# Kernel optimization log

Measured on AMD Instinct MI355X. Metric: run time of the kernel, lower is better.

The kernel has to match this reference:

```python
import math
import jax, jax.numpy as jnp
import numpy as np
from jax.scipy.special import erf

BATCH, SEQ, DIM = 2, 4096, 128
EMA_HEADS, DQK, DV = 16, 64, 256
NUM_BUCKETS, MAX_DIST = 32, 128


def _next_fast_len(n):
    # smallest 5-smooth integer >= n (matches scipy.fftpack.next_fast_len)
    while True:
        m = n
        for p in (2, 3, 5):
            while m % p == 0:
                m //= p
        if m == 1:
            return n
        n += 1


def _laplacian_attn(x):
    mu = math.sqrt(0.5)
    std = math.sqrt(0.25 * math.pi)
    return 0.5 * (1.0 + erf((x - mu) / (std * math.sqrt(2.0))))


def _rel_pos_bias(table, n, scale):
    # causal T5 relative position bias, bucket(q_pos - k_pos)
    pos = jnp.arange(n)
    rel = jnp.maximum(pos[:, None] - pos[None, :], 0)  # [n, n], >= 0
    max_exact = NUM_BUCKETS // 2
    is_small = rel < max_exact
    val_large = max_exact + (
        jnp.log(jnp.maximum(rel, 1).astype(jnp.float32) / max_exact)
        / math.log(MAX_DIST / max_exact) * (NUM_BUCKETS - max_exact)
    ).astype(jnp.int32)
    val_large = jnp.minimum(val_large, NUM_BUCKETS - 1)
    bucket = jnp.where(is_small, rel, val_large)
    return table[bucket, 0] * scale  # [n, n]


def _conv1d_fft(x, K, n):
    # x: [b, n, h, d] (fft over axis 1), K: [n, h] (fft over axis 0)
    fast_len = _next_fast_len(2 * n - 1)
    f_x = jnp.fft.rfft(x, n=fast_len, axis=1)
    f_K = jnp.fft.rfft(K, n=fast_len, axis=0)
    out = jnp.fft.irfft(f_x * jnp.conj(f_K)[None, :, :, None], fast_len, axis=1)
    out = jnp.roll(out, -1, axis=1)
    return out[:, fast_len - n:]  # [b, n, h, d]


def _forward(x, expansion, reduction, alphas, dampen, Wqk, bqk, gamma, beta,
             Wv, bv, rel_table, Wr, br, Wu, bu, Wh, Uh, bh):
    b, n, d = x.shape
    # ---- multi-headed EMA (causal -> unidirectional) via FFT conv ----
    xe = jnp.einsum('bnd,hd->bnhd', x, expansion)
    a = jax.nn.sigmoid(alphas)            # [h]
    dm = jax.nn.sigmoid(dampen)           # [h]
    powers = jnp.arange(n - 1, -1, -1, dtype=x.dtype)  # reversed powers
    K = a * ((1.0 - a) * dm) ** powers[:, None]        # [n, h]
    conv = _conv1d_fft(xe, K, n)
    ema = jnp.einsum('bnhd,hd->bnd', conv, reduction)  # [b, n, d]
    # ---- single-headed attention (chunk_size=-1 -> one chunk), v from x ----
    qk = jax.nn.silu(ema @ Wqk + bqk)     # [b, n, dqk]
    q = qk * gamma[0] + beta[0]
    k = qk * gamma[1] + beta[1]
    v = jax.nn.silu(x @ Wv + bv)          # [b, n, dv]
    scale = 1.0 / n                       # laplacian_attn_fn scaling
    sim = jnp.einsum('bid,bjd->bij', q, k) * scale
    sim = sim + _rel_pos_bias(rel_table, n, DQK ** 0.5)
    attn = _laplacian_attn(sim)
    causal_mask = jnp.triu(jnp.ones((n, n), dtype=bool), 1)
    attn = jnp.where(causal_mask, 0.0, attn)  # laplacian: zero after activation
    attn_out = jnp.einsum('bij,bjd->bid', attn, v)  # [b, n, dv]
    # ---- gating + output ----
    reset_gate = jax.nn.silu(ema @ Wr + br)         # [b, n, dv]
    update_gate = jax.nn.sigmoid(ema @ Wu + bu)     # [b, n, d]
    gated = attn_out * reset_gate
    H = jax.nn.silu(ema @ Wh + gated @ Uh + bh)     # [b, n, d]
    return update_gate * H + (1.0 - update_gate) * x


def setup_inputs() -> dict:
    key = jax.random.key(0)
    ks = jax.random.split(key, 18)
    def rn(i, shape, s=1.0):
        return jax.random.normal(ks[i], shape, dtype=jnp.float32) * s
    return dict(
        x=rn(0, (BATCH, SEQ, DIM)),
        expansion=rn(1, (EMA_HEADS, DIM), 0.2),
        reduction=rn(2, (EMA_HEADS, DIM), 0.2),
        alphas=rn(3, (EMA_HEADS,)),
        dampen=rn(4, (EMA_HEADS,)),
        Wqk=rn(5, (DIM, DQK), 0.05), bqk=rn(6, (DQK,), 0.02),
        gamma=rn(7, (2, DQK), 0.02), beta=jnp.zeros((2, DQK), jnp.float32),
        Wv=rn(8, (DIM, DV), 0.05), bv=rn(9, (DV,), 0.02),
        rel_table=rn(10, (NUM_BUCKETS, 1), 0.02),
        Wr=rn(11, (DIM, DV), 0.05), br=rn(12, (DV,), 0.02),
        Wu=rn(13, (DIM, DIM), 0.05), bu=rn(14, (DIM,), 0.02),
        Wh=rn(15, (DIM, DIM), 0.05), Uh=rn(16, (DV, DIM), 0.05),
        bh=rn(17, (DIM,), 0.02),
    )


def reference(x, expansion, reduction, alphas, dampen, Wqk, bqk, gamma, beta,
              Wv, bv, rel_table, Wr, br, Wu, bu, Wh, Uh, bh):
    return _forward(x, expansion, reduction, alphas, dampen, Wqk, bqk, gamma,
                    beta, Wv, bv, rel_table, Wr, br, Wu, bu, Wh, Uh, bh)
```

## Files before the change

kernel.cpp:

```cpp
#include <hip/hip_runtime.h>
#include <cstdint>
#include <cmath>

#define B_ 2
#define N_ 4096
#define D_ 128
#define H_ 16
#define DQK_ 64
#define DV_ 256

typedef float    f4_t  __attribute__((ext_vector_type(4)));
typedef float    f16f  __attribute__((ext_vector_type(16)));
typedef _Float16 h4_t  __attribute__((ext_vector_type(4)));
typedef _Float16 h8_t  __attribute__((ext_vector_type(8)));

__device__ __forceinline__ float sigmoidf_(float z) { return 1.f/(1.f + expf(-z)); }
__device__ __forceinline__ float siluf_(float z)    { return z/(1.f + expf(-z)); }
__device__ __forceinline__ f16f zero16() {
  f16f z;
#pragma unroll
  for (int i = 0; i < 16; ++i) z[i] = 0.f;
  return z;
}

__global__ void ema_phase1(const float* __restrict__ x, const float* __restrict__ expansion,
                           const float* __restrict__ alphas, const float* __restrict__ dampen,
                           float* __restrict__ F, _Float16* __restrict__ xh) {
  int bid = blockIdx.x;
  int dg = bid & 7, c = (bid >> 3) & 63, b = bid >> 9;
  int h = threadIdx.x & 15, dl = threadIdx.x >> 4;
  int d = dg*16 + dl;
  float a  = sigmoidf_(alphas[h]);
  float dm = sigmoidf_(dampen[h]);
  float q  = (1.f - a)*dm;
  float coef = a * expansion[h*D_ + d];
  __shared__ float xs[64][16];
  {
    int e = threadIdx.x;
    int t = e >> 2, seg = e & 3;
    const float* xp = x + ((size_t)b*N_ + c*64 + t)*D_ + dg*16 + seg*4;
    f4_t v = *(const f4_t*)xp;
    *(f4_t*)&xs[t][seg*4] = v;
    h4_t hv;
#pragma unroll
    for (int j = 0; j < 4; ++j) hv[j] = (_Float16)v[j];
    *(h4_t*)(xh + ((size_t)b*N_ + c*64 + t)*D_ + dg*16 + seg*4) = hv;
  }
  __syncthreads();
  float s = 0.f;
#pragma unroll
  for (int t = 0; t < 64; ++t) s = fmaf(q, s, coef*xs[t][dl]);
  F[(((size_t)b*H_ + h)*D_ + d)*64 + c] = s;
}

__global__ void ema_carry(const float* __restrict__ F, const float* __restrict__ alphas,
                          const float* __restrict__ dampen, float* __restrict__ carry) {
  int idx = blockIdx.x*256 + threadIdx.x;
  int h = (idx >> 7) & 15;
  float a  = sigmoidf_(alphas[h]);
  float dm = sigmoidf_(dampen[h]);
  float q  = (1.f - a)*dm;
  float qL = q;
#pragma unroll
  for (int i = 0; i < 6; ++i) qL *= qL;
  const float* Fp = F + (size_t)idx*64;
  float* cp = carry + (size_t)idx*64;
  float s = 0.f;
  for (int cc = 0; cc < 64; ++cc) { cp[cc] = s; s = fmaf(qL, s, Fp[cc]); }
}

__global__ void ema_phase2(const float* __restrict__ x, const float* __restrict__ expansion,
                           const float* __restrict__ reduction,
                           const float* __restrict__ alphas, const float* __restrict__ dampen,
                           const float* __restrict__ carry, _Float16* __restrict__ emah) {
  int bid = blockIdx.x;
  int dg = bid & 7, c = (bid >> 3) & 63, b = bid >> 9;
  int h = threadIdx.x & 15, dl = threadIdx.x >> 4;
  int d = dg*16 + dl;
  float a  = sigmoidf_(alphas[h]);
  float dm = sigmoidf_(dampen[h]);
  float q  = (1.f - a)*dm;
  float coef = a * expansion[h*D_ + d];
  float red  = reduction[h*D_ + d];
  __shared__ float xs[64][16];
  {
    int e = threadIdx.x;
    int t = e >> 2, seg = e & 3;
    const float* xp = x + ((size_t)b*N_ + c*64 + t)*D_ + dg*16 + seg*4;
    *(f4_t*)&xs[t][seg*4] = *(const f4_t*)xp;
  }
  __syncthreads();
  float s = carry[(((size_t)b*H_ + h)*D_ + d)*64 + c];
  for (int t = 0; t < 64; ++t) {
    s = fmaf(q, s, coef*xs[t][dl]);
    float v = red * s;
    v += __shfl_xor(v, 1); v += __shfl_xor(v, 2);
    v += __shfl_xor(v, 4); v += __shfl_xor(v, 8);
    if (h == 0) emah[((size_t)b*N_ + c*64 + t)*D_ + d] = (_Float16)v;
  }
}

__global__ void prep_all(const float* __restrict__ Wqk, const float* __restrict__ Wv,
                         const float* __restrict__ Wr, const float* __restrict__ Wu,
                         const float* __restrict__ Wh,
                         const float* __restrict__ bqk, const float* __restrict__ bv,
                         const float* __restrict__ br, const float* __restrict__ bu,
                         const float* __restrict__ bh,
                         const float* __restrict__ Uh, const float* __restrict__ rel_table,
                         _Float16* __restrict__ Wt, float* __restrict__ bcat,
                         _Float16* __restrict__ Uht, float* __restrict__ bias2T) {
  int idx = blockIdx.x*256 + threadIdx.x;
  if (idx < 832*128) {
    int c = idx >> 7, d = idx & 127;
    const float* W; const float* bias; int ncol, cl;
    if (c < 64)       { W=Wqk; bias=bqk; ncol=64;  cl=c; }
    else if (c < 320) { W=Wv;  bias=bv;  ncol=256; cl=c-64; }
    else if (c < 576) { W=Wr;  bias=br;  ncol=256; cl=c-320; }
    else if (c < 704) { W=Wu;  bias=bu;  ncol=128; cl=c-576; }
    else              { W=Wh;  bias=bh;  ncol=128; cl=c-704; }
    Wt[idx] = (_Float16)W[d*ncol + cl];
    if (d == 0) bcat[c] = bias[cl];
  } else if (idx < 832*128 + 32768) {
    int i2 = idx - 832*128;
    int k = i2 >> 7, c = i2 & 127;
    Uht[(size_t)c*256 + k] = (_Float16)Uh[i2];
  } else if (idx < 832*128 + 32768 + 4096) {
    int r = idx - (832*128 + 32768);
    int bucket;
    if (r < 16) bucket = r;
    else {
      double v = log((double)r / 16.0) / log(8.0) * 16.0;
      bucket = 16 + (int)v;
      if (bucket > 31) bucket = 31;
    }
    bias2T[r] = (rel_table[bucket]*8.0f - 0.70710678f) * 1.1283792f;
  }
}

__global__ __launch_bounds__(256) void linear_mfma(
    const _Float16* __restrict__ emah, const _Float16* __restrict__ xh,
    const _Float16* __restrict__ Wt, const float* __restrict__ bcat,
    const float* __restrict__ gamma, const float* __restrict__ beta,
    _Float16* __restrict__ qh, _Float16* __restrict__ kh, _Float16* __restrict__ vTt,
    float* __restrict__ resetb, float* __restrict__ updateb, float* __restrict__ hemab) {
  int slab = blockIdx.x % 13, rt = blockIdx.x / 13;
  int tid = threadIdx.x;
  int lane = tid & 63, w = tid >> 6;
  int lr = lane & 15, lg = lane >> 4;
  int mode = (slab==0)?0:(slab<5)?1:(slab<9)?2:(slab<11)?3:4;
  const _Float16* src = (mode==1) ? xh : emah;
  __shared__ _Float16 As[64][136];
  __shared__ _Float16 Ws[64][136];
  {
    const h8_t* s8 = (const h8_t*)(src + (size_t)rt*64*D_);
#pragma unroll
    for (int i = 0; i < 4; ++i) {
      int idx = tid + i*256;
      int row = idx >> 4, seg = idx & 15;
      *(h8_t*)&As[row][seg*8] = s8[idx];
    }
    const h8_t* w8 = (const h8_t*)(Wt + (size_t)slab*64*D_);
#pragma unroll
    for (int i = 0; i < 4; ++i) {
      int idx = tid + i*256;
      int row = idx >> 4, seg = idx & 15;
      *(h8_t*)&Ws[row][seg*8] = w8[idx];
    }
  }
  __syncthreads();
  h4_t af[8];
#pragma unroll
  for (int ks = 0; ks < 8; ++ks) af[ks] = *(const h4_t*)&As[w*16 + lr][ks*16 + lg*4];
  int row0 = rt*64 + w*16 + lg*4;
#pragma unroll
  for (int ns = 0; ns < 4; ++ns) {
    f4_t acc = (f4_t){0.f,0.f,0.f,0.f};
#pragma unroll
    for (int ks = 0; ks < 8; ++ks) {
      h4_t bf = *(const h4_t*)&Ws[ns*16 + lr][ks*16 + lg*4];
      acc = __builtin_amdgcn_mfma_f32_16x16x16f16(af[ks], bf, acc, 0, 0, 0);
    }
    int c = slab*64 + ns*16 + lr;
    float bias = bcat[c];
    if (mode == 0) {
      float g0 = gamma[c], g1 = gamma[64+c], be0 = beta[c], be1 = beta[64+c];
#pragma unroll
      for (int r = 0; r < 4; ++r) {
        float qk = siluf_(acc[r] + bias);
        size_t row = row0 + r;
        qh[row*DQK_ + c] = (_Float16)(qk*g0 + be0);
        kh[row*DQK_ + c] = (_Float16)(qk*g1 + be1);
      }
    } else if (mode == 1) {
      int cl = c - 64;
      int bb = row0 >> 12, rl = row0 & 4095;
      h4_t vv;
#pragma unroll
      for (int r = 0; r < 4; ++r) vv[r] = (_Float16)siluf_(acc[r] + bias);
      *(h4_t*)&vTt[(((size_t)bb*128 + (rl>>5))*256 + cl)*32 + (rl&31)] = vv;
    } else if (mode == 2) {
      int cl = c - 320;
#pragma unroll
      for (int r = 0; r < 4; ++r) resetb[(size_t)(row0 + r)*DV_ + cl] = siluf_(acc[r] + bias);
    } else if (mode == 3) {
      int cl = c - 576;
#pragma unroll
      for (int r = 0; r < 4; ++r) updateb[(size_t)(row0 + r)*D_ + cl] = sigmoidf_(acc[r] + bias);
    } else {
      int cl = c - 704;
#pragma unroll
      for (int r = 0; r < 4; ++r) hemab[(size_t)(row0 + r)*D_ + cl] = acc[r] + bias;
    }
  }
}

__global__ __launch_bounds__(256, 3) void attn_kernel(
    const _Float16* __restrict__ qh, const _Float16* __restrict__ kh,
    const _Float16* __restrict__ vTt, const float* __restrict__ bias2T,
    float* __restrict__ attnp) {
  int bid = blockIdx.x;
  int b = bid & 1;
  int s = (bid >> 1) & 7;
  int it = 63 - (bid >> 4);
  int q_ = it >> 3, r_ = it & 7;
  int nblk = q_ + 1;
  if (s >= nblk) return;
  int slot = 4*q_*(q_+1) + r_*(q_+1) + s;
  int i0 = it * 64;
  int jlo = 16*s;
  int jhi = min(16*s + 16, 2*it + 2);
  int nt = jhi - jlo;
  int tid = threadIdx.x;
  int lane = tid & 63, w = tid >> 6;
  int ih = w & 1, dvh = w >> 1;
  int lm = lane & 31, lg = lane >> 5;

  __shared__ __align__(16) char lds[2][22784];
  __shared__ float biasW[576];

  int jmax = jhi*32 - 1, jmin = jlo*32;
  int dlo = i0 - jmax;
  int cnt = 64 + jmax - jmin;
  for (int k = tid; k < cnt; k += 256) {
    int d = dlo + k;
    biasW[k] = d < 0 ? -1e38f : bias2T[d];
  }

  h4_t qf[8];
  {
    const _Float16* qp = qh + ((size_t)b*N_ + i0 + ih*32 + lm)*DQK_ + 4*lg;
#pragma unroll
    for (int ksq = 0; ksq < 8; ++ksq) qf[ksq] = *(const h4_t*)(qp + 8*ksq);
  }

  f16f accO[4];
#pragma unroll
  for (int i = 0; i < 4; ++i) accO[i] = zero16();

  const _Float16* kbase = kh + (size_t)b*N_*DQK_;
  const _Float16* vbase = vTt + (size_t)b*128*8192;
  int kj = tid >> 3, kseg = tid & 7;

  h8_t k8r, vreg[4];
#define ISSUE_(JT) { \
  k8r = *(const h8_t*)(kbase + (size_t)((JT)*32 + kj)*DQK_ + kseg*8); \
  const _Float16* vp_ = vbase + (size_t)(JT)*8192 + tid*32; \
  _Pragma("unroll") for (int i = 0; i < 4; ++i) vreg[i] = *(const h8_t*)(vp_ + i*8); }

#define COMMIT_(BUF) { \
  char* buf_ = (BUF); \
  char* ka_ = buf_ + kj*136 + kseg*16; \
  *(h4_t*)ka_ = __builtin_shufflevector(k8r, k8r, 0,1,2,3); \
  *(h4_t*)(ka_ + 8) = __builtin_shufflevector(k8r, k8r, 4,5,6,7); \
  char* va_ = buf_ + 4352 + tid*72; \
  _Pragma("unroll") for (int i = 0; i < 4; ++i) { \
    *(h4_t*)(va_ + i*16) = __builtin_shufflevector(vreg[i], vreg[i], 0,1,2,3); \
    *(h4_t*)(va_ + i*16 + 8) = __builtin_shufflevector(vreg[i], vreg[i], 4,5,6,7); } }

  ISSUE_(jlo); COMMIT_(lds[0]);
  if (nt > 1) ISSUE_(jlo + 1);
  __syncthreads();

  const float C1 = 1.1283792f / 4096.f;
  int ibase = i0 + ih*32 + lm;
#pragma unroll 1
  for (int t = 0; t < nt; ++t) {
    const char* kb = lds[t & 1];
    const char* vb = lds[t & 1] + 4352;
    __builtin_amdgcn_s_setprio(1);
    f16f accS = zero16();
#pragma unroll
    for (int ksq = 0; ksq < 8; ++ksq) {
      h4_t kf = *(const h4_t*)(kb + lm*136 + 16*ksq + 8*lg);
      accS = __builtin_amdgcn_mfma_f32_32x32x8f16(kf, qf[ksq], accS, 0, 0, 0);
    }
    __builtin_amdgcn_s_setprio(0);
    h4_t pa[4];
    {
      int idx0 = ibase - dlo - (jlo + t)*32 - 4*lg;
#pragma unroll
      for (int rr = 0; rr < 16; ++rr) {
        float tt = fmaf(accS[rr], C1, biasW[idx0 - 8*(rr>>2) - (rr&3)]);
        float e = tt*fmaf(tt*tt, -0.101797f, -2.304877f);
        float u = exp2f(e);
        float pv = __builtin_amdgcn_rcpf(1.f + u);
        pa[rr>>2][rr&3] = (_Float16)pv;
      }
    }
    __builtin_amdgcn_s_setprio(1);
#pragma unroll
    for (int ks = 0; ks < 4; ++ks) {
#pragma unroll
      for (int dvb = 0; dvb < 4; ++dvb) {
        h4_t vf = *(const h4_t*)(vb + (dvh*128 + dvb*32 + lm)*72 + 16*ks + 8*lg);
        accO[dvb] = __builtin_amdgcn_mfma_f32_32x32x8f16(pa[ks], vf, accO[dvb], 0, 0, 0);
      }
    }
    __builtin_amdgcn_s_setprio(0);
    if (t+1 < nt) COMMIT_(lds[(t+1) & 1]);
    if (t+2 < nt) ISSUE_(jlo + t + 2);
    __syncthreads();
  }
#undef ISSUE_
#undef COMMIT_

  float* op = attnp + ((size_t)b*288 + slot)*(64*256);
#pragma unroll
  for (int dvb = 0; dvb < 4; ++dvb) {
    int col = dvh*128 + dvb*32 + lm;
#pragma unroll
    for (int rr = 0; rr < 16; ++rr) {
      int row = ih*32 + 8*(rr>>2) + 4*lg + (rr&3);
      op[(size_t)row*256 + col] = accO[dvb][rr];
    }
  }
}

__global__ void combine_gated(const float* __restrict__ attnp, const float* __restrict__ resetb,
                              _Float16* __restrict__ gatedh) {
  size_t fi = (size_t)blockIdx.x*256 + threadIdx.x;
  int c4 = (int)(fi & 63);
  int rr = (int)(fi >> 6);
  int b = rr >> 12, n = rr & 4095;
  int it = n >> 6, rowLocal = n & 63;
  int q_ = it >> 3, r_ = it & 7;
  int nblk = q_ + 1;
  int base = 4*q_*(q_+1) + r_*(q_+1);
  const f4_t* ap = (const f4_t*)(attnp + (((size_t)b*288 + base)*64 + rowLocal)*256);
  f4_t acc = (f4_t){0.f,0.f,0.f,0.f};
  for (int s = 0; s < nblk; ++s)
    acc += ap[(size_t)s*4096 + c4];
  f4_t rg = ((const f4_t*)resetb)[fi];
  f4_t g = acc * rg;
  h4_t hg;
#pragma unroll
  for (int j = 0; j < 4; ++j) hg[j] = (_Float16)g[j];
  *(h4_t*)(gatedh + fi*4) = hg;
}

__global__ __launch_bounds__(256) void final_mfma(
    const _Float16* __restrict__ gatedh, const _Float16* __restrict__ Uht,
    const float* __restrict__ hemab, const float* __restrict__ updateb,
    const float* __restrict__ x, float* __restrict__ out) {
  int rt = blockIdx.x >> 1, cs = blockIdx.x & 1;
  int tid = threadIdx.x;
  int lane = tid & 63, w = tid >> 6;
  int lr = lane & 15, lg = lane >> 4;
  int row0 = rt*64, c0 = cs*64;
  __shared__ _Float16 As[64][136];
  __shared__ _Float16 Ws[64][136];
  f4_t acc[4];
#pragma unroll
  for (int ns = 0; ns < 4; ++ns) acc[ns] = (f4_t){0.f,0.f,0.f,0.f};
#pragma unroll
  for (int kc = 0; kc < 2; ++kc) {
    __syncthreads();
#pragma unroll
    for (int i = 0; i < 4; ++i) {
      int idx = tid + i*256;
      int row = idx >> 4, seg = idx & 15;
      *(h8_t*)&As[row][seg*8] =
          *(const h8_t*)(gatedh + (size_t)(row0 + row)*DV_ + kc*128 + seg*8);
      *(h8_t*)&Ws[row][seg*8] =
          *(const h8_t*)(Uht + (size_t)(c0 + row)*DV_ + kc*128 + seg*8);
    }
    __syncthreads();
    h4_t af[8];
#pragma unroll
    for (int ks = 0; ks < 8; ++ks) af[ks] = *(const h4_t*)&As[w*16 + lr][ks*16 + lg*4];
#pragma unroll
    for (int ns = 0; ns < 4; ++ns) {
#pragma unroll
      for (int ks = 0; ks < 8; ++ks) {
        h4_t bf = *(const h4_t*)&Ws[ns*16 + lr][ks*16 + lg*4];
        acc[ns] = __builtin_amdgcn_mfma_f32_16x16x16f16(af[ks], bf, acc[ns], 0, 0, 0);
      }
    }
  }
  int orow = row0 + w*16 + lg*4;
#pragma unroll
  for (int ns = 0; ns < 4; ++ns) {
    int col = c0 + ns*16 + lr;
#pragma unroll
    for (int r = 0; r < 4; ++r) {
      size_t o = (size_t)(orow + r)*D_ + col;
      float z = acc[ns][r] + hemab[o];
      float Hv = siluf_(z);
      float u  = updateb[o];
      out[o] = u*Hv + (1.f - u)*x[o];
    }
  }
}

extern "C" void kernel_launch(void* const* d_in, const int* in_sizes, int n_in,
                              void* d_out, int out_size, void* d_ws, size_t ws_size,
                              hipStream_t stream) {
  (void)in_sizes; (void)n_in; (void)out_size; (void)ws_size;
  const float* x         = (const float*)d_in[0];
  const float* expansion = (const float*)d_in[1];
  const float* reduction = (const float*)d_in[2];
  const float* alphas    = (const float*)d_in[3];
  const float* dampen    = (const float*)d_in[4];
  const float* Wqk       = (const float*)d_in[5];
  const float* bqk       = (const float*)d_in[6];
  const float* gamma     = (const float*)d_in[7];
  const float* beta      = (const float*)d_in[8];
  const float* Wv        = (const float*)d_in[9];
  const float* bv        = (const float*)d_in[10];
  const float* rel_table = (const float*)d_in[11];
  const float* Wr        = (const float*)d_in[12];
  const float* br        = (const float*)d_in[13];
  const float* Wu        = (const float*)d_in[14];
  const float* bu        = (const float*)d_in[15];
  const float* Wh        = (const float*)d_in[16];
  const float* Uh        = (const float*)d_in[17];
  const float* bh        = (const float*)d_in[18];
  float* out = (float*)d_out;

  char* p = (char*)d_ws;
  size_t off = 0;
  auto alloc = [&](size_t bytes) -> char* {
    char* r = p + off;
    off += (bytes + 255) & ~(size_t)255;
    return r;
  };
  float*    F      = (float*)alloc((size_t)B_*H_*D_*64*4);
  float*    carry  = (float*)alloc((size_t)B_*H_*D_*64*4);
  _Float16* emah   = (_Float16*)alloc((size_t)B_*N_*D_*2);
  _Float16* xh     = (_Float16*)alloc((size_t)B_*N_*D_*2);
  float*    bias2T = (float*)alloc((size_t)N_*4);
  _Float16* Wt     = (_Float16*)alloc((size_t)832*128*2);
  float*    bcat   = (float*)alloc((size_t)832*4);
  _Float16* Uht    = (_Float16*)alloc((size_t)D_*DV_*2);
  _Float16* qh     = (_Float16*)alloc((size_t)B_*N_*DQK_*2);
  _Float16* kh     = (_Float16*)alloc((size_t)B_*N_*DQK_*2);
  _Float16* vTt    = (_Float16*)alloc((size_t)B_*DV_*N_*2);
  float*    resetb = (float*)alloc((size_t)B_*N_*DV_*4);
  float*    updateb= (float*)alloc((size_t)B_*N_*D_*4);
  float*    hemab  = (float*)alloc((size_t)B_*N_*D_*4);
  _Float16* gatedh = (_Float16*)alloc((size_t)B_*N_*DV_*2);
  float*    attnp  = (float*)alloc((size_t)B_*288*64*DV_*4);

  prep_all<<<560, 256, 0, stream>>>(Wqk, Wv, Wr, Wu, Wh, bqk, bv, br, bu, bh,
                                    Uh, rel_table, Wt, bcat, Uht, bias2T);
  ema_phase1<<<1024, 256, 0, stream>>>(x, expansion, alphas, dampen, F, xh);
  ema_carry<<<16, 256, 0, stream>>>(F, alphas, dampen, carry);
  ema_phase2<<<1024, 256, 0, stream>>>(x, expansion, reduction, alphas, dampen, carry, emah);
  linear_mfma<<<128*13, 256, 0, stream>>>(emah, xh, Wt, bcat, gamma, beta,
                                          qh, kh, vTt, resetb, updateb, hemab);
  attn_kernel<<<1024, 256, 0, stream>>>(qh, kh, vTt, bias2T, attnp);
  combine_gated<<<2048, 256, 0, stream>>>(attnp, resetb, gatedh);
  final_mfma<<<256, 256, 0, stream>>>(gatedh, Uht, hemab, updateb, x, out);
}
```

Measured before the change: 121.5 us.

## Rebalance attention split-K into finer even splits and store fp16 partials

The causal attention work split changes from fixed 16-tile key chunks (up to 8 splits per query tile) to up to 16 splits per query tile, with key tiles divided evenly among splits. The grid doubles and per-block work becomes more uniform, which is meant to shrink tail imbalance and raise occupancy. Partial outputs are now written and read as fp16 instead of fp32, halving partial-buffer traffic in the attention and combine kernels. The risks are extra combine reads from more partials and some precision loss from fp16 partial sums.

```diff
diff --git a/kernel.cpp b/kernel.cpp
--- a/kernel.cpp
+++ b/kernel.cpp
@@ -217,28 +217,29 @@
 __global__ __launch_bounds__(256, 3) void attn_kernel(
     const _Float16* __restrict__ qh, const _Float16* __restrict__ kh,
     const _Float16* __restrict__ vTt, const float* __restrict__ bias2T,
-    float* __restrict__ attnp) {
+    _Float16* __restrict__ attnp) {
   int bid = blockIdx.x;
-  int b = bid & 1;
-  int s = (bid >> 1) & 7;
-  int it = 63 - (bid >> 4);
-  int q_ = it >> 3, r_ = it & 7;
-  int nblk = q_ + 1;
+  int it = 63 - (bid >> 5);
+  int rem = bid & 31;
+  int s = rem >> 1, b = rem & 1;
+  int a = it >> 2, r = it & 3;
+  int nblk = a + 1;
   if (s >= nblk) return;
-  int slot = 4*q_*(q_+1) + r_*(q_+1) + s;
+  int T = 2*it + 2;
+  int tlo = (s*T)/nblk, thi = ((s+1)*T)/nblk;
+  int nt = thi - tlo;
+  int base = it + 2*a*(a-1) + r*a;
+  int slot = base + s;
   int i0 = it * 64;
-  int jlo = 16*s;
-  int jhi = min(16*s + 16, 2*it + 2);
-  int nt = jhi - jlo;
   int tid = threadIdx.x;
   int lane = tid & 63, w = tid >> 6;
   int ih = w & 1, dvh = w >> 1;
   int lm = lane & 31, lg = lane >> 5;
 
   __shared__ __align__(16) char lds[2][22784];
-  __shared__ float biasW[576];
-
-  int jmax = jhi*32 - 1, jmin = jlo*32;
+  __shared__ float biasW[320];
+
+  int jmax = thi*32 - 1, jmin = tlo*32;
   int dlo = i0 - jmax;
   int cnt = 64 + jmax - jmin;
   for (int k = tid; k < cnt; k += 256) {
@@ -277,8 +278,8 @@
     *(h4_t*)(va_ + i*16) = __builtin_shufflevector(vreg[i], vreg[i], 0,1,2,3); \
     *(h4_t*)(va_ + i*16 + 8) = __builtin_shufflevector(vreg[i], vreg[i], 4,5,6,7); } }
 
-  ISSUE_(jlo); COMMIT_(lds[0]);
-  if (nt > 1) ISSUE_(jlo + 1);
+  ISSUE_(tlo); COMMIT_(lds[0]);
+  if (nt > 1) ISSUE_(tlo + 1);
   __syncthreads();
 
   const float C1 = 1.1283792f / 4096.f;
@@ -297,7 +298,7 @@
     __builtin_amdgcn_s_setprio(0);
     h4_t pa[4];
     {
-      int idx0 = ibase - dlo - (jlo + t)*32 - 4*lg;
+      int idx0 = ibase - dlo - (tlo + t)*32 - 4*lg;
 #pragma unroll
       for (int rr = 0; rr < 16; ++rr) {
         float tt = fmaf(accS[rr], C1, biasW[idx0 - 8*(rr>>2) - (rr&3)]);
@@ -318,38 +319,41 @@
     }
     __builtin_amdgcn_s_setprio(0);
     if (t+1 < nt) COMMIT_(lds[(t+1) & 1]);
-    if (t+2 < nt) ISSUE_(jlo + t + 2);
+    if (t+2 < nt) ISSUE_(tlo + t + 2);
     __syncthreads();
   }
 #undef ISSUE_
 #undef COMMIT_
 
-  float* op = attnp + ((size_t)b*288 + slot)*(64*256);
+  _Float16* op = attnp + ((size_t)b*544 + slot)*(64*256);
 #pragma unroll
   for (int dvb = 0; dvb < 4; ++dvb) {
     int col = dvh*128 + dvb*32 + lm;
 #pragma unroll
     for (int rr = 0; rr < 16; ++rr) {
       int row = ih*32 + 8*(rr>>2) + 4*lg + (rr&3);
-      op[(size_t)row*256 + col] = accO[dvb][rr];
-    }
-  }
-}
-
-__global__ void combine_gated(const float* __restrict__ attnp, const float* __restrict__ resetb,
+      op[(size_t)row*256 + col] = (_Float16)accO[dvb][rr];
+    }
+  }
+}
+
+__global__ void combine_gated(const _Float16* __restrict__ attnp, const float* __restrict__ resetb,
                               _Float16* __restrict__ gatedh) {
   size_t fi = (size_t)blockIdx.x*256 + threadIdx.x;
   int c4 = (int)(fi & 63);
   int rr = (int)(fi >> 6);
   int b = rr >> 12, n = rr & 4095;
   int it = n >> 6, rowLocal = n & 63;
-  int q_ = it >> 3, r_ = it & 7;
-  int nblk = q_ + 1;
-  int base = 4*q_*(q_+1) + r_*(q_+1);
-  const f4_t* ap = (const f4_t*)(attnp + (((size_t)b*288 + base)*64 + rowLocal)*256);
+  int a = it >> 2, r = it & 3;
+  int nblk = a + 1;
+  int base = it + 2*a*(a-1) + r*a;
+  const _Float16* ap = attnp + ((size_t)b*544 + base)*16384 + rowLocal*256 + c4*4;
   f4_t acc = (f4_t){0.f,0.f,0.f,0.f};
-  for (int s = 0; s < nblk; ++s)
-    acc += ap[(size_t)s*4096 + c4];
+  for (int s2 = 0; s2 < nblk; ++s2) {
+    h4_t pv = *(const h4_t*)(ap + (size_t)s2*16384);
+#pragma unroll
+    for (int j = 0; j < 4; ++j) acc[j] += (float)pv[j];
+  }
   f4_t rg = ((const f4_t*)resetb)[fi];
   f4_t g = acc * rg;
   h4_t hg;
@@ -459,7 +463,7 @@
   float*    updateb= (float*)alloc((size_t)B_*N_*D_*4);
   float*    hemab  = (float*)alloc((size_t)B_*N_*D_*4);
   _Float16* gatedh = (_Float16*)alloc((size_t)B_*N_*DV_*2);
-  float*    attnp  = (float*)alloc((size_t)B_*288*64*DV_*4);
+  _Float16* attnp  = (_Float16*)alloc((size_t)B_*544*64*256*2);
 
   prep_all<<<560, 256, 0, stream>>>(Wqk, Wv, Wr, Wu, Wh, bqk, bv, br, bu, bh,
                                     Uh, rel_table, Wt, bcat, Uht, bias2T);
@@ -468,7 +472,7 @@
   ema_phase2<<<1024, 256, 0, stream>>>(x, expansion, reduction, alphas, dampen, carry, emah);
   linear_mfma<<<128*13, 256, 0, stream>>>(emah, xh, Wt, bcat, gamma, beta,
                                           qh, kh, vTt, resetb, updateb, hemab);
-  attn_kernel<<<1024, 256, 0, stream>>>(qh, kh, vTt, bias2T, attnp);
+  attn_kernel<<<2048, 256, 0, stream>>>(qh, kh, vTt, bias2T, attnp);
   combine_gated<<<2048, 256, 0, stream>>>(attnp, resetb, gatedh);
   final_mfma<<<256, 256, 0, stream>>>(gatedh, Uht, hemab, updateb, x, out);
 }
```

Measured after the change: 120.3 us. About the same (-1.0%).
